# Performance work log

Hardware: AMD Instinct MI355X
Metric: run time of the kernel (lower is better)

Reference implementation:

```python
import jax, jax.numpy as jnp
import numpy as np
import math

B, S, D, H, DK = 4, 2048, 512, 8, 64

def _xavier(key, shape):
    fan_in, fan_out = shape[-2], shape[-1]
    std = math.sqrt(2.0 / (fan_in + fan_out))
    return jax.random.normal(key, shape, dtype=jnp.float32) * std

def setup_inputs() -> dict:
    key = jax.random.key(0)
    ks = jax.random.split(key, 5)
    X = jax.random.normal(ks[0], (B, S, D), dtype=jnp.float32)
    W_q = _xavier(ks[1], (H, D, DK))
    W_k = _xavier(ks[2], (H, D, DK))
    W_v = _xavier(ks[3], (H, D, DK))
    W_o = _xavier(ks[4], (H * DK, D))
    return {"X": X, "W_q": W_q, "W_k": W_k, "W_v": W_v, "W_o": W_o}

def reference(X, W_q, W_k, W_v, W_o):
    d_k = W_q.shape[-1]
    # project all heads at once: [B,H,S,dk]
    Q = jnp.einsum('bsd,hdk->bhsk', X, W_q)
    K = jnp.einsum('bsd,hdk->bhsk', X, W_k)
    V = jnp.einsum('bsd,hdk->bhsk', X, W_v)
    scores = jnp.einsum('bhsk,bhtk->bhst', Q, K) / jnp.sqrt(jnp.asarray(d_k, X.dtype))
    seq_len = X.shape[1]
    causal = jnp.tril(jnp.ones((seq_len, seq_len), dtype=bool))  # strict upper -> -inf
    scores = jnp.where(causal[None, None, :, :], scores, -jnp.inf)
    attn = jax.nn.softmax(scores, axis=-1)
    out = jnp.einsum('bhst,bhtk->bhsk', attn, V)  # [B,H,S,dv]
    # original concat order: permute to (B,S,dv,H) then flatten -> head axis fastest
    Bx, Hx, Sx, DV = out.shape
    concat = jnp.transpose(out, (0, 2, 3, 1)).reshape(Bx, Sx, DV * Hx)
    return jnp.matmul(concat, W_o)
```

## Files before the change

### kernel.cpp

```cpp
#include <hip/hip_runtime.h>
#include <hip/hip_bf16.h>


typedef __bf16 bf16;
typedef __bf16 bf16x8 __attribute__((ext_vector_type(8)));
typedef __bf16 bf16x4 __attribute__((ext_vector_type(4)));
typedef __bf16 bf16x2 __attribute__((ext_vector_type(2)));
typedef float  f32x4  __attribute__((ext_vector_type(4)));
typedef float  f32x16 __attribute__((ext_vector_type(16)));
typedef unsigned int u32;
typedef u32 u32x4 __attribute__((ext_vector_type(4)));

#define AS1 __attribute__((address_space(1)))
#define AS3 __attribute__((address_space(3)))

__device__ __forceinline__ void async_lds16(const void* gsrc, void* ldst) {
  __builtin_amdgcn_global_load_lds((AS1 const void*)gsrc, (AS3 void*)ldst, 16, 0, 0);
}

__device__ __forceinline__ float fexp2(float x) {
  float r;
  asm("v_exp_f32 %0, %1" : "=v"(r) : "v"(x));
  return r;
}


__global__ __launch_bounds__(256) void k_cvt_all(const float4* __restrict__ X4,
                                                 const float* __restrict__ Wq,
                                                 const float* __restrict__ Wk,
                                                 const float* __restrict__ Wv,
                                                 const float* __restrict__ Wo,
                                                 bf16x4* __restrict__ Xb4,
                                                 bf16* __restrict__ BT,
                                                 bf16* __restrict__ WoT) {
  int t = blockIdx.x * 256 + threadIdx.x;
  if (t < 1048576) {
    float4 v = X4[t];
    bf16x4 o = { (bf16)v.x, (bf16)v.y, (bf16)v.z, (bf16)v.w };
    Xb4[t] = o;
  } else {
    int u = t - 1048576;
    if (u < 786432) {
      int n = u >> 9, d = u & 511;
      int which = n >> 9, h = (n >> 6) & 7, dk = n & 63;
      const float* W = (which == 0) ? Wq : ((which == 1) ? Wk : Wv);
      BT[u] = (bf16)W[((h << 9) + d) * 64 + dk];
    } else {
      int i2 = u - 786432;
      int d = i2 >> 9, c = i2 & 511;
      int h = c >> 6, dk = c & 63;
      WoT[i2] = (bf16)Wo[(((dk << 3) + h) << 9) + d];
    }
  }
}


__device__ __forceinline__ void gemm_tile(const bf16* __restrict__ A,
                                          const bf16* __restrict__ BT,
                                          int K, int m0, int n0,
                                          char* sm, f32x4 acc[4][4]) {
  const int tid = threadIdx.x;
  const int lane = tid & 63, w = tid >> 6;
  const int wm = w >> 1, wn = w & 1;
  const int lr = lane & 15, lg = lane >> 4;
#define GSTAGE(bi, k0) do {                                                        \
    char* base_ = sm + ((bi) << 14);                                               \
    _Pragma("unroll")                                                              \
    for (int i_ = 0; i_ < 2; ++i_) {                                               \
      int off_ = i_ * 256 + tid;                                                   \
      int row_ = off_ >> 2, cb_ = (off_ & 3) << 4;                                 \
      async_lds16((const char*)(A  + (m0 + row_) * K + (k0)) + cb_,                \
                  base_ + off_ * 16);                                              \
      async_lds16((const char*)(BT + (n0 + row_) * K + (k0)) + cb_,                \
                  base_ + 8192 + off_ * 16);                                       \
    }                                                                              \
  } while (0)
  const int NT = K >> 5;
  GSTAGE(0, 0);
  asm volatile("s_waitcnt vmcnt(0)" ::: "memory");
  __builtin_amdgcn_s_barrier();
  __builtin_amdgcn_sched_barrier(0);
  for (int t = 0; t < NT; ++t) {
    char* cb = sm + ((t & 1) << 14);
    if (t + 1 < NT) GSTAGE((t + 1) & 1, (t + 1) << 5);
    bf16x8 af[4], bfr[4];
    #pragma unroll
    for (int u = 0; u < 4; ++u) {
      af[u]  = *(const bf16x8*)(cb +        ((wm * 64 + u * 16 + lr) * 32 + 8 * lg) * 2);
      bfr[u] = *(const bf16x8*)(cb + 8192 + ((wn * 64 + u * 16 + lr) * 32 + 8 * lg) * 2);
    }
    __builtin_amdgcn_s_setprio(1);
    #pragma unroll
    for (int am = 0; am < 4; ++am)
      #pragma unroll
      for (int bn = 0; bn < 4; ++bn)
        acc[am][bn] = __builtin_amdgcn_mfma_f32_16x16x32_bf16(af[am], bfr[bn], acc[am][bn], 0, 0, 0);
    __builtin_amdgcn_s_setprio(0);
    if (t + 1 < NT) {
      asm volatile("s_waitcnt vmcnt(0)" ::: "memory");
      __builtin_amdgcn_s_barrier();
      __builtin_amdgcn_sched_barrier(0);
    }
  }
#undef GSTAGE
}

__global__ __launch_bounds__(256) void k_gemm_qkv(const bf16* __restrict__ A,
                                                  const bf16* __restrict__ BT,
                                                  bf16* __restrict__ Qb,
                                                  bf16* __restrict__ Kb,
                                                  bf16* __restrict__ VTb) {
  __shared__ char sm[32768];
  const int m0 = blockIdx.y * 128, n0 = blockIdx.x * 128;
  f32x4 acc[4][4];
  #pragma unroll
  for (int a = 0; a < 4; ++a)
    #pragma unroll
    for (int b = 0; b < 4; ++b) { f32x4 z = {0.f,0.f,0.f,0.f}; acc[a][b] = z; }
  gemm_tile(A, BT, 512, m0, n0, sm, acc);
  const int lane = threadIdx.x & 63, w = threadIdx.x >> 6;
  const int wm = w >> 1, wn = w & 1, lr = lane & 15, lg = lane >> 4;
  const float qsc = 0.1803368801f;
  #pragma unroll
  for (int am = 0; am < 4; ++am)
    #pragma unroll
    for (int bn = 0; bn < 4; ++bn)
      #pragma unroll
      for (int r = 0; r < 4; ++r) {
        int m = m0 + wm * 64 + am * 16 + 4 * lg + r;
        int n = n0 + wn * 64 + bn * 16 + lr;
        int b = m >> 11, s = m & 2047;
        int which = n >> 9, h = (n >> 6) & 7, dk = n & 63;
        int bh = (b << 3) + h;
        float x = acc[am][bn][r];
        if (which == 0)      Qb[((bh << 11) + s) * 64 + dk] = (bf16)(x * qsc);
        else if (which == 1) Kb[((bh << 11) + s) * 64 + dk] = (bf16)x;
        else                 VTb[((bh << 6) + dk) * 2048 + s] = (bf16)x;
      }
}

__global__ __launch_bounds__(256) void k_gemm_out(const bf16* __restrict__ A,
                                                  const bf16* __restrict__ BT,
                                                  float* __restrict__ C) {
  __shared__ char sm[24576];
  const int m0 = blockIdx.y * 128, n0 = blockIdx.x * 64;
  const int tid = threadIdx.x;
  const int lane = tid & 63, w = tid >> 6;
  const int wm = w >> 1, wn = w & 1;
  const int lr = lane & 15, lg = lane >> 4;
  f32x4 acc[4][2];
  #pragma unroll
  for (int a = 0; a < 4; ++a)
    #pragma unroll
    for (int b = 0; b < 2; ++b) { f32x4 z = {0.f,0.f,0.f,0.f}; acc[a][b] = z; }
#define GSTAGE2(bi, k0) do {                                                       \
    char* base_ = sm + (bi) * 12288;                                               \
    _Pragma("unroll")                                                              \
    for (int i_ = 0; i_ < 2; ++i_) {                                               \
      int off_ = i_ * 256 + tid;                                                   \
      int row_ = off_ >> 2, cb_ = (off_ & 3) << 4;                                 \
      async_lds16((const char*)(A + (m0 + row_) * 512 + (k0)) + cb_,               \
                  base_ + off_ * 16);                                              \
    }                                                                              \
    {                                                                              \
      int off_ = tid;                                                              \
      int row_ = off_ >> 2, cb_ = (off_ & 3) << 4;                                 \
      async_lds16((const char*)(BT + (n0 + row_) * 512 + (k0)) + cb_,              \
                  base_ + 8192 + off_ * 16);                                       \
    }                                                                              \
  } while (0)
  GSTAGE2(0, 0);
  asm volatile("s_waitcnt vmcnt(0)" ::: "memory");
  __builtin_amdgcn_s_barrier();
  __builtin_amdgcn_sched_barrier(0);
  for (int t = 0; t < 16; ++t) {
    char* cb = sm + (t & 1) * 12288;
    if (t + 1 < 16) GSTAGE2((t + 1) & 1, (t + 1) << 5);
    bf16x8 af[4], bfr[2];
    #pragma unroll
    for (int u = 0; u < 4; ++u)
      af[u] = *(const bf16x8*)(cb + ((wm * 64 + u * 16 + lr) * 32 + 8 * lg) * 2);
    #pragma unroll
    for (int v = 0; v < 2; ++v)
      bfr[v] = *(const bf16x8*)(cb + 8192 + ((wn * 32 + v * 16 + lr) * 32 + 8 * lg) * 2);
    __builtin_amdgcn_s_setprio(1);
    #pragma unroll
    for (int am = 0; am < 4; ++am)
      #pragma unroll
      for (int bn = 0; bn < 2; ++bn)
        acc[am][bn] = __builtin_amdgcn_mfma_f32_16x16x32_bf16(af[am], bfr[bn], acc[am][bn], 0, 0, 0);
    __builtin_amdgcn_s_setprio(0);
    if (t + 1 < 16) {
      asm volatile("s_waitcnt vmcnt(0)" ::: "memory");
      __builtin_amdgcn_s_barrier();
      __builtin_amdgcn_sched_barrier(0);
    }
  }
#undef GSTAGE2
  #pragma unroll
  for (int am = 0; am < 4; ++am)
    #pragma unroll
    for (int bn = 0; bn < 2; ++bn)
      #pragma unroll
      for (int r = 0; r < 4; ++r) {
        int m = m0 + wm * 64 + am * 16 + 4 * lg + r;
        int n = n0 + wn * 32 + bn * 16 + lr;
        C[(m << 9) + n] = acc[am][bn][r];
      }
}


__device__ __forceinline__ void attn_stage(char* base, const bf16* Kh, const bf16* Vh,
                                           int tb, int tid) {
  #pragma unroll
  for (int k = 0; k < 2; ++k) {
    int s = tid + (k << 8);
    int row = s >> 3, g = s & 7;
    async_lds16((const void*)(Kh + ((tb + row) << 6) + ((g ^ (row & 7)) << 3)),
                base + s * 16);
  }
  #pragma unroll
  for (int k = 0; k < 2; ++k) {
    int s = tid + (k << 8);
    int row = s >> 3, g = s & 7;
    async_lds16((const void*)(Vh + (row << 11) + tb + ((g ^ (row & 7)) << 3)),
                base + 8192 + s * 16);
  }
}

__global__ __launch_bounds__(256, 2) void k_attn6(const bf16* __restrict__ Qb,
                                                  const bf16* __restrict__ Kb,
                                                  const bf16* __restrict__ VTb,
                                                  bf16* __restrict__ Oc) {
  __shared__ char sm[32768];
  const int tid = threadIdx.x, lane = tid & 63, wv = tid >> 6;
  const int l31 = lane & 31, hi = lane >> 5;
  const int bid = blockIdx.x;
  const int bh = bid & 31;
  const int qb = (bid < 256) ? (15 - (bid >> 5)) : ((bid - 256) >> 5);
  const int b = bh >> 3, h = bh & 7;
  const int q0 = qb << 7;
  const int wq0 = q0 + (wv << 5);
  const bf16* Qh = Qb  + ((size_t)bh << 17);
  const bf16* Kh = Kb  + ((size_t)bh << 17);
  const bf16* Vh = VTb + ((size_t)bh << 17);

  bf16x8 qf[4];
  #pragma unroll
  for (int kd = 0; kd < 4; ++kd)
    qf[kd] = *(const bf16x8*)(Qh + ((wq0 + l31) << 6) + kd * 16 + 8 * hi);

  f32x16 o0, o1;
  #pragma unroll
  for (int r = 0; r < 16; ++r) { o0[r] = 0.f; o1[r] = 0.f; }
  float m_run = -3e38f, lsum = 0.f;

  const int NT = (qb << 1) + 2;
  const int swz = l31 & 7;

  attn_stage(sm, Kh, Vh, 0, tid);

  for (int t = 0; t < NT; ++t) {
    const int tb = t << 6;
    char* cb = sm + ((t & 1) << 14);
    __syncthreads();
    if (t + 1 < NT)
      attn_stage(sm + (((t + 1) & 1) << 14), Kh, Vh, (t + 1) << 6, tid);
    if (tb > wq0 + 31) continue;

    f32x16 sA, sB;
    #pragma unroll
    for (int r = 0; r < 16; ++r) { sA[r] = 0.f; sB[r] = 0.f; }
    {
      bf16x8 kf[4];
      #pragma unroll
      for (int kd = 0; kd < 4; ++kd)
        kf[kd] = *(const bf16x8*)(cb + l31 * 128 + ((((kd << 1) + hi) ^ swz) << 4));
      __builtin_amdgcn_s_setprio(1);
      #pragma unroll
      for (int kd = 0; kd < 4; ++kd)
        sA = __builtin_amdgcn_mfma_f32_32x32x16_bf16(kf[kd], qf[kd], sA, 0, 0, 0);
      __builtin_amdgcn_s_setprio(0);
      #pragma unroll
      for (int kd = 0; kd < 4; ++kd)
        kf[kd] = *(const bf16x8*)(cb + (32 + l31) * 128 + ((((kd << 1) + hi) ^ swz) << 4));
      __builtin_amdgcn_s_setprio(1);
      #pragma unroll
      for (int kd = 0; kd < 4; ++kd)
        sB = __builtin_amdgcn_mfma_f32_32x32x16_bf16(kf[kd], qf[kd], sB, 0, 0, 0);
      __builtin_amdgcn_s_setprio(0);
    }

    const int sg = wq0 + l31;
    if (tb + 63 > wq0) {
      #pragma unroll
      for (int r = 0; r < 16; ++r) {
        int rk = tb + (r & 3) + 8 * (r >> 2) + 4 * hi;
        sA[r] = (rk > sg)      ? -1e30f : sA[r];
        sB[r] = (rk + 32 > sg) ? -1e30f : sB[r];
      }
    }
    float tv[16];
    #pragma unroll
    for (int r = 0; r < 16; ++r) tv[r] = fmaxf(sA[r], sB[r]);
    float m0_ = fmaxf(tv[0], tv[1]),  m1_ = fmaxf(tv[2], tv[3]);
    float m2_ = fmaxf(tv[4], tv[5]),  m3_ = fmaxf(tv[6], tv[7]);
    float m4_ = fmaxf(tv[8], tv[9]),  m5_ = fmaxf(tv[10], tv[11]);
    float m6_ = fmaxf(tv[12], tv[13]), m7_ = fmaxf(tv[14], tv[15]);
    float tmax = fmaxf(fmaxf(fmaxf(m0_, m1_), fmaxf(m2_, m3_)),
                       fmaxf(fmaxf(m4_, m5_), fmaxf(m6_, m7_)));
    float tms = fmaxf(tmax, __shfl_xor(tmax, 32));
    if (!__all(tms <= m_run + 8.f)) {
      float mn = fmaxf(m_run, tms);
      float fac = fexp2(m_run - mn);
      #pragma unroll
      for (int r = 0; r < 16; ++r) { o0[r] *= fac; o1[r] *= fac; }
      lsum *= fac;
      m_run = mn;
    }
    #pragma unroll
    for (int r = 0; r < 16; ++r) sA[r] = fexp2(sA[r] - m_run);
    #pragma unroll
    for (int r = 0; r < 16; ++r) sB[r] = fexp2(sB[r] - m_run);
    float a0 = (sA[0]+sB[0]) + (sA[1]+sB[1]),   a1 = (sA[2]+sB[2]) + (sA[3]+sB[3]);
    float a2 = (sA[4]+sB[4]) + (sA[5]+sB[5]),   a3 = (sA[6]+sB[6]) + (sA[7]+sB[7]);
    float a4 = (sA[8]+sB[8]) + (sA[9]+sB[9]),   a5 = (sA[10]+sB[10]) + (sA[11]+sB[11]);
    float a6 = (sA[12]+sB[12]) + (sA[13]+sB[13]), a7 = (sA[14]+sB[14]) + (sA[15]+sB[15]);
    float rs = ((a0 + a1) + (a2 + a3)) + ((a4 + a5) + (a6 + a7));
    lsum += rs + __shfl_xor(rs, 32);

    #pragma unroll
    for (int j = 0; j < 2; ++j) {
      u32 pk_[8];
      #pragma unroll
      for (int i = 0; i < 8; ++i) {
        float plo = j ? sB[2 * i] : sA[2 * i];
        float phi = j ? sB[2 * i + 1] : sA[2 * i + 1];
        bf16x2 pr = { (bf16)plo, (bf16)phi };
        pk_[i] = __builtin_bit_cast(u32, pr);
      }
      asm volatile("v_permlane32_swap_b32 %0, %1" : "+v"(pk_[0]), "+v"(pk_[2]));
      asm volatile("v_permlane32_swap_b32 %0, %1" : "+v"(pk_[1]), "+v"(pk_[3]));
      asm volatile("v_permlane32_swap_b32 %0, %1" : "+v"(pk_[4]), "+v"(pk_[6]));
      asm volatile("v_permlane32_swap_b32 %0, %1" : "+v"(pk_[5]), "+v"(pk_[7]));
      u32x4 w0 = { pk_[0], pk_[1], pk_[2], pk_[3] };
      u32x4 w1 = { pk_[4], pk_[5], pk_[6], pk_[7] };
      bf16x8 pb0 = __builtin_bit_cast(bf16x8, w0);
      bf16x8 pb1 = __builtin_bit_cast(bf16x8, w1);
      const char* vb = cb + 8192;
      bf16x8 v00 = *(const bf16x8*)(vb + l31 * 128        + ((((j << 2) + hi) ^ swz) << 4));
      bf16x8 v01 = *(const bf16x8*)(vb + l31 * 128        + ((((j << 2) + 2 + hi) ^ swz) << 4));
      bf16x8 v10 = *(const bf16x8*)(vb + (32 + l31) * 128 + ((((j << 2) + hi) ^ swz) << 4));
      bf16x8 v11 = *(const bf16x8*)(vb + (32 + l31) * 128 + ((((j << 2) + 2 + hi) ^ swz) << 4));
      __builtin_amdgcn_s_setprio(1);
      o0 = __builtin_amdgcn_mfma_f32_32x32x16_bf16(v00, pb0, o0, 0, 0, 0);
      o0 = __builtin_amdgcn_mfma_f32_32x32x16_bf16(v01, pb1, o0, 0, 0, 0);
      o1 = __builtin_amdgcn_mfma_f32_32x32x16_bf16(v10, pb0, o1, 0, 0, 0);
      o1 = __builtin_amdgcn_mfma_f32_32x32x16_bf16(v11, pb1, o1, 0, 0, 0);
      __builtin_amdgcn_s_setprio(0);
    }
  }

  float rn = 1.f / lsum;
  const int sg = wq0 + l31;
  bf16* Orow = Oc + (((size_t)((b << 11) + sg)) << 9) + (h << 6);
  #pragma unroll
  for (int g = 0; g < 4; ++g) {
    bf16x4 v0, v1;
    #pragma unroll
    for (int i = 0; i < 4; ++i) {
      v0[i] = (bf16)(o0[4 * g + i] * rn);
      v1[i] = (bf16)(o1[4 * g + i] * rn);
    }
    *(bf16x4*)(Orow + 4 * hi + 8 * g)      = v0;
    *(bf16x4*)(Orow + 32 + 4 * hi + 8 * g) = v1;
  }
}


extern "C" void kernel_launch(void* const* d_in, const int* in_sizes, int n_in,
                              void* d_out, int out_size, void* d_ws, size_t ws_size,
                              hipStream_t stream) {
  (void)in_sizes; (void)n_in; (void)out_size; (void)ws_size;
  const float* X  = (const float*)d_in[0];
  const float* Wq = (const float*)d_in[1];
  const float* Wk = (const float*)d_in[2];
  const float* Wv = (const float*)d_in[3];
  const float* Wo = (const float*)d_in[4];
  float* out = (float*)d_out;
  char* ws = (char*)d_ws;
  bf16* Xb   = (bf16*)(ws);
  bf16* Wqkv = (bf16*)(ws + 8388608);
  bf16* WoT  = (bf16*)(ws + 9961472);
  bf16* Qb   = (bf16*)(ws + 10485760);
  bf16* Kb   = (bf16*)(ws + 18874368);
  bf16* VTb  = (bf16*)(ws + 27262976);
  bf16* Oc   = (bf16*)(ws + 35651584);

  k_cvt_all<<<8192, 256, 0, stream>>>((const float4*)X, Wq, Wk, Wv, Wo,
                                      (bf16x4*)Xb, Wqkv, WoT);
  k_gemm_qkv<<<dim3(12, 64), 256, 0, stream>>>(Xb, Wqkv, Qb, Kb, VTb);
  k_attn6<<<512, 256, 0, stream>>>(Qb, Kb, VTb, Oc);
  k_gemm_out<<<dim3(8, 64), 256, 0, stream>>>(Oc, WoT, out);
}
```

Before: 92.18 us.

## Triple-buffer LDS staging with partial vmcnt waits in GEMM and attention

Switches the double-buffered async global-to-LDS pipelines in the QKV GEMM, output GEMM and attention kernels to three-stage buffers. Loads run two tiles ahead, and each iteration waits only for the older tile via partial vmcnt counts rather than draining all loads. This is meant to hide global memory latency behind MFMA work and drops one barrier per iteration. The cost is 50% more LDS per block, which may lower occupancy, especially for the attention kernel that asks for 2 blocks per CU. The partial-wait counts also have to match the exact number of loads issued per stage.

Measured after the change: 98.15 us. 1.06x slower.

```diff
diff --git a/kernel.cpp b/kernel.cpp
--- a/kernel.cpp
+++ b/kernel.cpp
@@ -64,7 +64,7 @@
   const int wm = w >> 1, wn = w & 1;
   const int lr = lane & 15, lg = lane >> 4;
 #define GSTAGE(bi, k0) do {                                                        \
-    char* base_ = sm + ((bi) << 14);                                               \
+    char* base_ = sm + (bi) * 16384;                                               \
     _Pragma("unroll")                                                              \
     for (int i_ = 0; i_ < 2; ++i_) {                                               \
       int off_ = i_ * 256 + tid;                                                   \
@@ -77,12 +77,17 @@
   } while (0)
   const int NT = K >> 5;
   GSTAGE(0, 0);
-  asm volatile("s_waitcnt vmcnt(0)" ::: "memory");
-  __builtin_amdgcn_s_barrier();
-  __builtin_amdgcn_sched_barrier(0);
+  if (NT > 1) GSTAGE(1, 32);
+  int cur = 0;
   for (int t = 0; t < NT; ++t) {
-    char* cb = sm + ((t & 1) << 14);
-    if (t + 1 < NT) GSTAGE((t + 1) & 1, (t + 1) << 5);
+    if (t + 1 < NT) asm volatile("s_waitcnt vmcnt(4)" ::: "memory");
+    else            asm volatile("s_waitcnt vmcnt(0)" ::: "memory");
+    __builtin_amdgcn_s_barrier();
+    if (t + 2 < NT) {
+      int nb = cur + 2; if (nb >= 3) nb -= 3;
+      GSTAGE(nb, (t + 2) << 5);
+    }
+    char* cb = sm + cur * 16384;
     bf16x8 af[4], bfr[4];
     #pragma unroll
     for (int u = 0; u < 4; ++u) {
@@ -96,11 +101,7 @@
       for (int bn = 0; bn < 4; ++bn)
         acc[am][bn] = __builtin_amdgcn_mfma_f32_16x16x32_bf16(af[am], bfr[bn], acc[am][bn], 0, 0, 0);
     __builtin_amdgcn_s_setprio(0);
-    if (t + 1 < NT) {
-      asm volatile("s_waitcnt vmcnt(0)" ::: "memory");
-      __builtin_amdgcn_s_barrier();
-      __builtin_amdgcn_sched_barrier(0);
-    }
+    cur = (cur == 2) ? 0 : cur + 1;
   }
 #undef GSTAGE
 }
@@ -110,7 +111,7 @@
                                                   bf16* __restrict__ Qb,
                                                   bf16* __restrict__ Kb,
                                                   bf16* __restrict__ VTb) {
-  __shared__ char sm[32768];
+  __shared__ char sm[49152];
   const int m0 = blockIdx.y * 128, n0 = blockIdx.x * 128;
   f32x4 acc[4][4];
   #pragma unroll
@@ -142,7 +143,7 @@
 __global__ __launch_bounds__(256) void k_gemm_out(const bf16* __restrict__ A,
                                                   const bf16* __restrict__ BT,
                                                   float* __restrict__ C) {
-  __shared__ char sm[24576];
+  __shared__ char sm[36864];
   const int m0 = blockIdx.y * 128, n0 = blockIdx.x * 64;
   const int tid = threadIdx.x;
   const int lane = tid & 63, w = tid >> 6;
@@ -170,12 +171,17 @@
     }                                                                              \
   } while (0)
   GSTAGE2(0, 0);
-  asm volatile("s_waitcnt vmcnt(0)" ::: "memory");
-  __builtin_amdgcn_s_barrier();
-  __builtin_amdgcn_sched_barrier(0);
+  GSTAGE2(1, 32);
+  int cur = 0;
   for (int t = 0; t < 16; ++t) {
-    char* cb = sm + (t & 1) * 12288;
-    if (t + 1 < 16) GSTAGE2((t + 1) & 1, (t + 1) << 5);
+    if (t + 1 < 16) asm volatile("s_waitcnt vmcnt(3)" ::: "memory");
+    else            asm volatile("s_waitcnt vmcnt(0)" ::: "memory");
+    __builtin_amdgcn_s_barrier();
+    if (t + 2 < 16) {
+      int nb = cur + 2; if (nb >= 3) nb -= 3;
+      GSTAGE2(nb, (t + 2) << 5);
+    }
+    char* cb = sm + cur * 12288;
     bf16x8 af[4], bfr[2];
     #pragma unroll
     for (int u = 0; u < 4; ++u)
@@ -190,11 +196,7 @@
       for (int bn = 0; bn < 2; ++bn)
         acc[am][bn] = __builtin_amdgcn_mfma_f32_16x16x32_bf16(af[am], bfr[bn], acc[am][bn], 0, 0, 0);
     __builtin_amdgcn_s_setprio(0);
-    if (t + 1 < 16) {
-      asm volatile("s_waitcnt vmcnt(0)" ::: "memory");
-      __builtin_amdgcn_s_barrier();
-      __builtin_amdgcn_sched_barrier(0);
-    }
+    cur = (cur == 2) ? 0 : cur + 1;
   }
 #undef GSTAGE2
   #pragma unroll
@@ -232,7 +234,7 @@
                                                   const bf16* __restrict__ Kb,
                                                   const bf16* __restrict__ VTb,
                                                   bf16* __restrict__ Oc) {
-  __shared__ char sm[32768];
+  __shared__ char sm[49152];
   const int tid = threadIdx.x, lane = tid & 63, wv = tid >> 6;
   const int l31 = lane & 31, hi = lane >> 5;
   const int bid = blockIdx.x;
@@ -259,13 +261,20 @@
   const int swz = l31 & 7;
 
   attn_stage(sm, Kh, Vh, 0, tid);
+  if (NT > 1) attn_stage(sm + 16384, Kh, Vh, 64, tid);
+  int cur = 0;
 
   for (int t = 0; t < NT; ++t) {
     const int tb = t << 6;
-    char* cb = sm + ((t & 1) << 14);
-    __syncthreads();
-    if (t + 1 < NT)
-      attn_stage(sm + (((t + 1) & 1) << 14), Kh, Vh, (t + 1) << 6, tid);
+    if (t + 1 < NT) asm volatile("s_waitcnt vmcnt(4)" ::: "memory");
+    else            asm volatile("s_waitcnt vmcnt(0)" ::: "memory");
+    __builtin_amdgcn_s_barrier();
+    if (t + 2 < NT) {
+      int nb = cur + 2; if (nb >= 3) nb -= 3;
+      attn_stage(sm + nb * 16384, Kh, Vh, (t + 2) << 6, tid);
+    }
+    char* cb = sm + cur * 16384;
+    cur = (cur == 2) ? 0 : cur + 1;
     if (tb > wq0 + 31) continue;
 
     f32x16 sA, sB;
```
